# Performance work log

Measured on AMD Instinct MI355X. Metric: run time of the kernel, lower is better.

Reference implementation:

```python
import jax, jax.numpy as jnp
import numpy as np

B, S, H, NH = 2, 2048, 2048, 16
HD = H // NH  # 128
NEG = -1e9


def _rope_tables(seq_len, dim, dtype):
    inv_freq = 1.0 / (10000.0 ** (jnp.arange(0, dim, 2, dtype=jnp.float32) / dim))
    t = jnp.arange(seq_len, dtype=jnp.float32)
    freqs = jnp.einsum('i,j->ij', t, inv_freq)          # [S, dim/2]
    emb = jnp.concatenate([freqs, freqs], axis=-1)      # [S, dim]
    return jnp.cos(emb).astype(dtype), jnp.sin(emb).astype(dtype)


def _rotate_half(x):
    x1, x2 = x[..., : x.shape[-1] // 2], x[..., x.shape[-1] // 2:]
    return jnp.concatenate([-x2, x1], axis=-1)


def setup_inputs() -> dict:
    key = jax.random.key(0)
    ks = jax.random.split(key, 5)
    hidden_states = jax.random.normal(ks[0], (B, S, H), dtype=jnp.float32)
    # causal additive mask [B, S, S]
    causal = jnp.where(jnp.tril(jnp.ones((S, S), dtype=bool)), 0.0, NEG).astype(jnp.float32)
    attention_mask = jnp.broadcast_to(causal, (B, S, S))
    sc = 1.0 / np.sqrt(H)
    Wq = jax.random.normal(ks[1], (H, H), dtype=jnp.float32) * sc
    Wk = jax.random.normal(ks[2], (H, H), dtype=jnp.float32) * sc
    Wv = jax.random.normal(ks[3], (H, H), dtype=jnp.float32) * sc
    Wo = jax.random.normal(ks[4], (H, H), dtype=jnp.float32) * sc
    return {"hidden_states": hidden_states, "attention_mask": attention_mask,
            "Wq": Wq, "Wk": Wk, "Wv": Wv, "Wo": Wo}


def reference(hidden_states, attention_mask, Wq, Wk, Wv, Wo):
    bsz, q_len, _ = hidden_states.shape
    dtype = hidden_states.dtype
    # QKV projections (nn.Linear: x @ W.T), split into heads -> [B, NH, S, HD]
    def proj(W):
        return jnp.einsum('bsh,dh->bsd', hidden_states, W).reshape(bsz, q_len, NH, HD).transpose(0, 2, 1, 3)
    q, k, v = proj(Wq), proj(Wk), proj(Wv)
    cos, sin = _rope_tables(q_len, HD, dtype)            # [S, HD]
    q = q * cos + _rotate_half(q) * sin
    k = k * cos + _rotate_half(k) * sin
    scaling = HD ** -0.5
    scores = jnp.einsum('bhqd,bhkd->bhqk', q, k) * scaling
    scores = scores + attention_mask[:, None, :, :]      # broadcast over heads
    attn = jax.nn.softmax(scores.astype(jnp.float32), axis=-1).astype(dtype)
    out = jnp.einsum('bhqk,bhkd->bhqd', attn, v)         # [B, NH, S, HD]
    out = out.transpose(0, 2, 1, 3).reshape(bsz, q_len, H)
    return jnp.einsum('bsh,dh->bsd', out, Wo)
```

## Files before the change

kernel.cpp:

```cpp
#include <hip/hip_runtime.h>
#include <hip/hip_bf16.h>
#include <math.h>

#define B_  2
#define S_  2048
#define H_  2048
#define NH_ 16
#define HD_ 128
#define M_  (B_*S_)

typedef __bf16 bf16_t;
typedef _Float16 f16_t;
typedef __bf16 bf16x8 __attribute__((ext_vector_type(8)));
typedef __bf16 bf16x4 __attribute__((ext_vector_type(4)));
typedef _Float16 f16x4 __attribute__((ext_vector_type(4)));
typedef float  f32x4  __attribute__((ext_vector_type(4)));

__device__ __forceinline__ f32x4 mfma_bf16_32(bf16x8 a, bf16x8 b, f32x4 c) {
  return __builtin_amdgcn_mfma_f32_16x16x32_bf16(a, b, c, 0, 0, 0);
}
__device__ __forceinline__ f32x4 mfma_f16_16(f16x4 a, f16x4 b, f32x4 c) {
  return __builtin_amdgcn_mfma_f32_16x16x16f16(a, b, c, 0, 0, 0);
}
__device__ __forceinline__ void gl_lds16(const void* g, void* l) {
  __builtin_amdgcn_global_load_lds((const __attribute__((address_space(1))) void*)g,
                                   (__attribute__((address_space(3))) void*)l, 16, 0, 0);
}
#define WAITCNT_VM(n) { asm volatile("" ::: "memory"); \
                        __builtin_amdgcn_s_waitcnt(((n) & 0xF) | 0x70 | 0xF00 | (((n) >> 4) << 14)); \
                        asm volatile("" ::: "memory"); }
#define BARRIER()     { asm volatile("" ::: "memory"); __builtin_amdgcn_s_barrier(); \
                        asm volatile("" ::: "memory"); }

__global__ void cvt_all(const float* __restrict__ hs, const float* __restrict__ wq,
                        const float* __restrict__ wk, const float* __restrict__ wv,
                        const float* __restrict__ wo, bf16_t* __restrict__ hs_b,
                        bf16_t* __restrict__ wqkv, bf16_t* __restrict__ wo_b) {
  int i = (blockIdx.x * 256 + threadIdx.x) * 4;
  const float* src;
  bf16_t* dst;
  if (i < 8388608)        { src = hs + i;              dst = hs_b + i; }
  else if (i < 12582912)  { src = wq + (i - 8388608);  dst = wqkv + (i - 8388608); }
  else if (i < 16777216)  { src = wk + (i - 12582912); dst = wqkv + (i - 8388608); }
  else if (i < 20971520)  { src = wv + (i - 16777216); dst = wqkv + (i - 8388608); }
  else                    { src = wo + (i - 20971520); dst = wo_b + (i - 20971520); }
  float4 v = *(const float4*)src;
  bf16x4 o;
  o[0] = (bf16_t)v.x; o[1] = (bf16_t)v.y; o[2] = (bf16_t)v.z; o[3] = (bf16_t)v.w;
  *(bf16x4*)dst = o;
}

template<int MODE>
__global__ __launch_bounds__(256, 3)
void gemm_mfma(const bf16_t* __restrict__ A, const bf16_t* __restrict__ Bt,
               bf16_t* __restrict__ outQ, bf16_t* __restrict__ outK,
               f16_t* __restrict__ outV, float* __restrict__ outF, int K) {
  __shared__ bf16_t sA[128 * 64];
  __shared__ bf16_t sB[128 * 64];
  const int tid  = threadIdx.x;
  const int lane = tid & 63;
  const int w    = tid >> 6;
  const int col  = lane & 15;
  const int quad = lane >> 4;
  const int w_m  = (w & 1) * 64;
  const int w_n  = (w >> 1) * 64;
  const int m_blk = blockIdx.y * 128;
  const int n_blk = blockIdx.x * 128;

  const int srow   = lane >> 3;
  const int schunk = (lane & 7) ^ (lane >> 3);

  const bf16_t* Abase = A  + (size_t)m_blk * K;
  const bf16_t* Bbase = Bt + (size_t)n_blk * K;

  f32x4 acc[4][4] = {};

  for (int kk = 0; kk < K; kk += 64) {
    __syncthreads();
#pragma unroll
    for (int p = 0; p < 4; ++p) {
      int seg = w * 4 + p;
      int row = seg * 8 + srow;
      gl_lds16(Abase + (size_t)row * K + kk + schunk * 8, &sA[seg * 512]);
      gl_lds16(Bbase + (size_t)row * K + kk + schunk * 8, &sB[seg * 512]);
    }
    __syncthreads();
#pragma unroll
    for (int kc = 0; kc < 2; ++kc) {
      bf16x8 af[4], bfr[4];
      const int cs = (kc * 4 + quad) ^ (col & 7);
#pragma unroll
      for (int i = 0; i < 4; ++i) {
        af[i]  = *(const bf16x8*)&sA[(w_m + i * 16 + col) * 64 + cs * 8];
        bfr[i] = *(const bf16x8*)&sB[(w_n + i * 16 + col) * 64 + cs * 8];
      }
#pragma unroll
      for (int mi = 0; mi < 4; ++mi)
#pragma unroll
        for (int ni = 0; ni < 4; ++ni)
          acc[mi][ni] = mfma_bf16_32(af[mi], bfr[ni], acc[mi][ni]);
    }
  }

  const int sel = n_blk >> 11;
  if (MODE == 0 && sel == 2) {
#pragma unroll
    for (int mi = 0; mi < 4; ++mi)
#pragma unroll
      for (int ni = 0; ni < 4; ++ni) {
        int m0 = m_blk + w_m + mi * 16 + quad * 4;
        int n  = n_blk + w_n + ni * 16 + col;
        int n_l = n & (H_ - 1);
        int head = n_l >> 7, hd = n_l & (HD_ - 1);
        int b = m0 >> 11, s0 = m0 & (S_ - 1);
        int bh = b * NH_ + head;
        int frag = (bh * 32 + (s0 >> 6)) * 32 + (hd >> 4) * 4 + ((s0 >> 4) & 3);
        int lane2 = ((s0 >> 2) & 3) * 16 + (hd & 15);
        f16x4 o;
#pragma unroll
        for (int r = 0; r < 4; ++r) o[r] = (f16_t)acc[mi][ni][r];
        *(f16x4*)&outV[(size_t)frag * 256 + lane2 * 4] = o;
      }
  } else {
#pragma unroll
    for (int mi = 0; mi < 4; ++mi)
#pragma unroll
      for (int ni = 0; ni < 4; ++ni)
#pragma unroll
        for (int r = 0; r < 4; ++r) {
          int m = m_blk + w_m + mi * 16 + quad * 4 + r;
          int n = n_blk + w_n + ni * 16 + col;
          float v = acc[mi][ni][r];
          if (MODE == 0) {
            int n_l = n & (H_ - 1);
            int head = n_l >> 7, hd = n_l & (HD_ - 1);
            int b = m >> 11, s = m & (S_ - 1);
            size_t idx = (((size_t)(b * NH_ + head)) * S_ + s) * HD_ + hd;
            if (sel == 0) outQ[idx] = (bf16_t)v;
            else          outK[idx] = (bf16_t)v;
          } else {
            outF[(size_t)m * H_ + n] = v;
          }
        }
  }
}

__global__ void rope_pack(bf16_t* __restrict__ Qb, const bf16_t* __restrict__ Kn,
                          bf16_t* __restrict__ Kp) {
  int i = blockIdx.x * 256 + threadIdx.x;
  int isK = i >> 19;
  int ii = i & 524287;
  int d8 = ii & 7;
  int s  = (ii >> 3) & (S_ - 1);
  int bh = ii >> 14;
  int d0 = d8 * 8;
  const bf16_t* row = (isK ? Kn : (const bf16_t*)Qb) + ((size_t)bh * S_ + s) * HD_;
  bf16x8 a = *(const bf16x8*)(row + d0);
  bf16x8 b = *(const bf16x8*)(row + d0 + 64);
  bf16x8 o1, o2;
#pragma unroll
  for (int j = 0; j < 8; ++j) {
    int d = d0 + j;
    float ang = (float)s * exp2f(-(float)d * (13.287712379549449f / 64.f));
    float c = cosf(ang), sn = sinf(ang);
    float x1 = (float)a[j], x2 = (float)b[j];
    o1[j] = (bf16_t)(x1 * c - x2 * sn);
    o2[j] = (bf16_t)(x2 * c + x1 * sn);
  }
  if (!isK) {
    bf16_t* wr = Qb + ((size_t)bh * S_ + s) * HD_;
    *(bf16x8*)(wr + d0)      = o1;
    *(bf16x8*)(wr + d0 + 64) = o2;
  } else {
    int kt = s >> 6, t = (s >> 4) & 3;
    int lane_ = (d8 & 3) * 16 + (s & 15);
    int kc1 = d0 >> 5;
    bf16_t* base = Kp + ((size_t)(bh * 32 + kt) * 16) * 512;
    *(bf16x8*)(base + (size_t)(t * 4 + kc1) * 512 + lane_ * 8)     = o1;
    *(bf16x8*)(base + (size_t)(t * 4 + kc1 + 2) * 512 + lane_ * 8) = o2;
  }
}

__global__ __launch_bounds__(256, 2)
void flash_attn(const bf16_t* __restrict__ Q, const bf16_t* __restrict__ Kp,
                const f16_t* __restrict__ Vp, bf16_t* __restrict__ Out) {
  __shared__ bf16_t sK[2][8192];
  __shared__ f16_t  sV[2][8192];
  const int lane = threadIdx.x & 63;
  const int col  = lane & 15;
  const int quad = lane >> 4;
  const int w    = threadIdx.x >> 6;

  const int c = blockIdx.x & 7, g = blockIdx.x >> 3;
  const int qt = (g == 0) ? c : (g == 1) ? 15 - c : (g == 2) ? 16 + c : 31 - c;
  const int bh = blockIdx.y;
  const int ktmax = qt;

  const bf16_t* KpB = Kp + (size_t)bh * 32 * 8192;
  const f16_t*  VpB = Vp + (size_t)bh * 32 * 8192;

  auto stage = [&](int kt, int p) {
#pragma unroll
    for (int r = 0; r < 4; ++r) {
      int seg = r * 4 + w;
      gl_lds16(KpB + (size_t)kt * 8192 + seg * 512 + lane * 8, &sK[p][seg * 512]);
      gl_lds16(VpB + (size_t)kt * 8192 + seg * 512 + lane * 8, &sV[p][seg * 512]);
    }
  };

  const float scale2 = 0.12751744154f;
  const bf16_t* Qrow = Q + ((size_t)bh * S_ + qt * 64 + w * 16 + col) * HD_;
  bf16x8 qf[4];
#pragma unroll
  for (int kc = 0; kc < 4; ++kc) {
    qf[kc] = *(const bf16x8*)(Qrow + kc * 32 + quad * 8);
#pragma unroll
    for (int j = 0; j < 8; ++j) qf[kc][j] = (bf16_t)((float)qf[kc][j] * scale2);
  }

  f32x4 oacc[8] = {};
  float m_i = -1e30f, l_i = 0.f;

  stage(0, 0);
  if (ktmax >= 1) stage(1, 1);
  if (ktmax >= 1) WAITCNT_VM(8) else WAITCNT_VM(0);
  BARRIER();

  for (int kt = 0; kt <= ktmax; ++kt) {
    const int p = kt & 1;

    f32x4 st[4] = {};
#pragma unroll
    for (int kc = 0; kc < 4; ++kc)
#pragma unroll
      for (int t = 0; t < 4; ++t) {
        bf16x8 kf = *(const bf16x8*)&sK[p][(t * 4 + kc) * 512 + lane * 8];
        st[t] = mfma_bf16_32(kf, qf[kc], st[t]);
      }

    if (kt == ktmax) {
      int ql = w * 16 + col;
#pragma unroll
      for (int t = 0; t < 4; ++t)
#pragma unroll
        for (int r = 0; r < 4; ++r)
          if (t * 16 + quad * 4 + r > ql) st[t][r] = -1e30f;
    }

    float mx = st[0][0];
#pragma unroll
    for (int t = 0; t < 4; ++t)
#pragma unroll
      for (int r = 0; r < 4; ++r) mx = fmaxf(mx, st[t][r]);
    mx = fmaxf(mx, __shfl_xor(mx, 16, 64));
    mx = fmaxf(mx, __shfl_xor(mx, 32, 64));
    float mn = fmaxf(m_i, mx);
    float alpha = 1.0f;
    if (__ballot(mx > m_i)) {
      alpha = exp2f(m_i - mn);
#pragma unroll
      for (int dt = 0; dt < 8; ++dt)
#pragma unroll
        for (int r = 0; r < 4; ++r) oacc[dt][r] *= alpha;
    }
    m_i = mn;

    float sum = 0.f;
    f16x4 pf[4];
#pragma unroll
    for (int t = 0; t < 4; ++t)
#pragma unroll
      for (int r = 0; r < 4; ++r) {
        float pv = exp2f(st[t][r] - mn);
        sum += pv;
        pf[t][r] = (f16_t)pv;
      }
    sum += __shfl_xor(sum, 16, 64);
    sum += __shfl_xor(sum, 32, 64);
    l_i = l_i * alpha + sum;

#pragma unroll
    for (int t = 0; t < 4; ++t)
#pragma unroll
      for (int dt = 0; dt < 8; ++dt) {
        f16x4 vf = *(const f16x4*)&sV[p][(dt * 4 + t) * 256 + lane * 4];
        oacc[dt] = mfma_f16_16(vf, pf[t], oacc[dt]);
      }

    if (kt < ktmax) {
      BARRIER();
      if (kt + 2 <= ktmax) {
        stage(kt + 2, p);
        WAITCNT_VM(8)
      } else {
        WAITCNT_VM(0)
      }
      BARRIER();
    }
  }

  float inv = 1.0f / l_i;
  int b = bh >> 4, h = bh & (NH_ - 1);
  int qg = qt * 64 + w * 16 + col;
  bf16_t* Orow = Out + ((size_t)b * S_ + qg) * H_ + h * HD_;
#pragma unroll
  for (int dt = 0; dt < 8; ++dt) {
    bf16x4 o4;
#pragma unroll
    for (int r = 0; r < 4; ++r) o4[r] = (bf16_t)(oacc[dt][r] * inv);
    *(bf16x4*)(Orow + dt * 16 + quad * 4) = o4;
  }
}

extern "C" void kernel_launch(void* const* d_in, const int* in_sizes, int n_in,
                              void* d_out, int out_size, void* d_ws, size_t ws_size,
                              hipStream_t stream) {
  const float* hs = (const float*)d_in[0];
  const float* Wq = (const float*)d_in[2];
  const float* Wk = (const float*)d_in[3];
  const float* Wv = (const float*)d_in[4];
  const float* Wo = (const float*)d_in[5];
  float* out = (float*)d_out;

  char* ws = (char*)d_ws;
  size_t off = 0;
  auto alloc = [&](size_t bytes) -> void* {
    void* p = ws + off;
    off += (bytes + 255) & ~(size_t)255;
    return p;
  };
  bf16_t* hs_b  = (bf16_t*)alloc((size_t)M_ * H_ * 2);
  bf16_t* wqkv  = (bf16_t*)alloc((size_t)3 * H_ * H_ * 2);
  bf16_t* wo_b  = (bf16_t*)alloc((size_t)H_ * H_ * 2);
  bf16_t* Qbuf  = (bf16_t*)alloc((size_t)M_ * H_ * 2);
  bf16_t* Kbuf  = (bf16_t*)alloc((size_t)M_ * H_ * 2);
  f16_t*  Vp    = (f16_t*)alloc((size_t)M_ * H_ * 2);
  bf16_t* attn  = (bf16_t*)alloc((size_t)M_ * H_ * 2);

  cvt_all<<<24576, 256, 0, stream>>>(hs, Wq, Wk, Wv, Wo, hs_b, wqkv, wo_b);

  gemm_mfma<0><<<dim3(48, 32), 256, 0, stream>>>(hs_b, wqkv, Qbuf, Kbuf,
                                                 Vp, nullptr, H_);

  bf16_t* Kp = wqkv;
  rope_pack<<<4096, 256, 0, stream>>>(Qbuf, Kbuf, Kp);

  flash_attn<<<dim3(32, 32), 256, 0, stream>>>(Qbuf, Kp, Vp, attn);

  gemm_mfma<1><<<dim3(16, 32), 256, 0, stream>>>(attn, wo_b, nullptr, nullptr,
                                                 nullptr, out, H_);
}
```

Baseline: 431.6 us.

## Single-buffer K/V in LDS with split staging to raise flash-attn occupancy

Replaces the double-buffered K/V LDS tiles with single buffers, halving shared memory, and raises launch bounds to 4 blocks per CU. K and V loads are now staged separately, so the next K tile is fetched during the PV matmul and the next V tile during the next QK step. MFMA sections are wrapped in s_setprio to favour matrix issue. The cost is extra barriers and less prefetch distance, which may expose load latency, and the register cap may cause spills.

```diff
diff --git a/kernel.cpp b/kernel.cpp
--- a/kernel.cpp
+++ b/kernel.cpp
@@ -181,11 +181,11 @@
   }
 }
 
-__global__ __launch_bounds__(256, 2)
+__global__ __launch_bounds__(256, 4)
 void flash_attn(const bf16_t* __restrict__ Q, const bf16_t* __restrict__ Kp,
                 const f16_t* __restrict__ Vp, bf16_t* __restrict__ Out) {
-  __shared__ bf16_t sK[2][8192];
-  __shared__ f16_t  sV[2][8192];
+  __shared__ bf16_t sK[8192];
+  __shared__ f16_t  sV[8192];
   const int lane = threadIdx.x & 63;
   const int col  = lane & 15;
   const int quad = lane >> 4;
@@ -199,12 +199,18 @@
   const bf16_t* KpB = Kp + (size_t)bh * 32 * 8192;
   const f16_t*  VpB = Vp + (size_t)bh * 32 * 8192;
 
-  auto stage = [&](int kt, int p) {
+  auto stageK = [&](int kt) {
 #pragma unroll
     for (int r = 0; r < 4; ++r) {
       int seg = r * 4 + w;
-      gl_lds16(KpB + (size_t)kt * 8192 + seg * 512 + lane * 8, &sK[p][seg * 512]);
-      gl_lds16(VpB + (size_t)kt * 8192 + seg * 512 + lane * 8, &sV[p][seg * 512]);
+      gl_lds16(KpB + (size_t)kt * 8192 + seg * 512 + lane * 8, &sK[seg * 512]);
+    }
+  };
+  auto stageV = [&](int kt) {
+#pragma unroll
+    for (int r = 0; r < 4; ++r) {
+      int seg = r * 4 + w;
+      gl_lds16(VpB + (size_t)kt * 8192 + seg * 512 + lane * 8, &sV[seg * 512]);
     }
   };
 
@@ -221,22 +227,22 @@
   f32x4 oacc[8] = {};
   float m_i = -1e30f, l_i = 0.f;
 
-  stage(0, 0);
-  if (ktmax >= 1) stage(1, 1);
-  if (ktmax >= 1) WAITCNT_VM(8) else WAITCNT_VM(0);
+  stageK(0);
+  stageV(0);
+  WAITCNT_VM(4)
   BARRIER();
 
   for (int kt = 0; kt <= ktmax; ++kt) {
-    const int p = kt & 1;
-
     f32x4 st[4] = {};
+    __builtin_amdgcn_s_setprio(1);
 #pragma unroll
     for (int kc = 0; kc < 4; ++kc)
 #pragma unroll
       for (int t = 0; t < 4; ++t) {
-        bf16x8 kf = *(const bf16x8*)&sK[p][(t * 4 + kc) * 512 + lane * 8];
+        bf16x8 kf = *(const bf16x8*)&sK[(t * 4 + kc) * 512 + lane * 8];
         st[t] = mfma_bf16_32(kf, qf[kc], st[t]);
       }
+    __builtin_amdgcn_s_setprio(0);
 
     if (kt == ktmax) {
       int ql = w * 16 + col;
@@ -279,22 +285,25 @@
     sum += __shfl_xor(sum, 32, 64);
     l_i = l_i * alpha + sum;
 
+    WAITCNT_VM(0)
+    BARRIER();
+
+    if (kt < ktmax) stageK(kt + 1);
+
+    __builtin_amdgcn_s_setprio(1);
 #pragma unroll
     for (int t = 0; t < 4; ++t)
 #pragma unroll
       for (int dt = 0; dt < 8; ++dt) {
-        f16x4 vf = *(const f16x4*)&sV[p][(dt * 4 + t) * 256 + lane * 4];
+        f16x4 vf = *(const f16x4*)&sV[(dt * 4 + t) * 256 + lane * 4];
         oacc[dt] = mfma_f16_16(vf, pf[t], oacc[dt]);
       }
+    __builtin_amdgcn_s_setprio(0);
 
     if (kt < ktmax) {
       BARRIER();
-      if (kt + 2 <= ktmax) {
-        stage(kt + 2, p);
-        WAITCNT_VM(8)
-      } else {
-        WAITCNT_VM(0)
-      }
+      stageV(kt + 1);
+      WAITCNT_VM(4)
       BARRIER();
     }
   }
```

After: 394.9 us. 1.09x faster.
